# Kernel tuning notes

Measured on AMD Instinct MI355X. Metric: run time of the kernel, lower is better.

The kernel has to match this reference:

```python
import jax, jax.numpy as jnp
import numpy as np

N_NODES = 50000
N_EDGES = 1_250_000
D = 64
L = 3

def setup_inputs() -> dict:
    key = jax.random.key(0)
    k1, k2, k3, k4, k5, k6 = jax.random.split(key, 6)
    h = jax.random.normal(k1, (N_NODES, D), dtype=jnp.float32)
    edge_weight = jax.random.uniform(k2, (N_EDGES,), dtype=jnp.float32)
    # Glorot-ish scale keeps tanh in its responsive range
    Ws = jax.random.normal(k3, (L, D, D), dtype=jnp.float32) * (1.0 / np.sqrt(D))
    bs = jax.random.normal(k4, (L, D), dtype=jnp.float32) * 0.01
    src = jax.random.randint(k5, (N_EDGES,), 0, N_NODES, dtype=jnp.int64 if jax.config.jax_enable_x64 else jnp.int32)
    dst = jax.random.randint(k6, (N_EDGES,), 0, N_NODES, dtype=jnp.int64 if jax.config.jax_enable_x64 else jnp.int32)
    return {"h": h, "edge_weight": edge_weight, "Ws": Ws, "bs": bs, "src": src, "dst": dst}

def reference(h, edge_weight, Ws, bs, src, dst):
    # Stacked DGL GraphConv(norm='none'), edge-weighted: aggregate-then-transform
    # (in_feats == out_feats, so DGL aggregates first), tanh between layers,
    # concat of all intermediate representations along feature dim.
    n = h.shape[0]
    results = [h]
    for i in range(L):
        msg = h[src] * edge_weight[:, None]            # [E, D] gather-scale
        agg = jax.ops.segment_sum(msg, dst, num_segments=n)  # [N, D] scatter-add
        h = agg @ Ws[i] + bs[i]                        # dense transform + bias
        if i != L - 1:
            h = jnp.tanh(h)
        results.append(h)
    return jnp.concatenate(results, axis=1)           # [N, (L+1)*D]
```

## Files before the change

kernel.cpp:

```cpp
#include <hip/hip_runtime.h>
#include <hip/hip_fp16.h>
#include <math.h>

#define N_NODES 50000
#define N_EDGES 1250000
#define D 64
#define OUTC 256
#define CAP 64
#define SCAN_BLOCKS ((N_NODES + 255) / 256)

#define WSB_CNT      0
#define WSB_BUCKET   802816
#define WSB_H16_0    13602816
#define WSB_H16_1    20002816
#define WS_BUCKET_NEEDED 26402816

#define WS_DEG      0
#define WS_FILL     204800
#define WS_ROWPTR   409600
#define WS_BSUM     609664
#define WS_BOFF     610496
#define WS_EDGES    614400
#define WS_H16_0    10616832
#define WS_H16_1    (WS_H16_0 + (size_t)N_NODES * D * 2)
#define WS_F16_NEEDED (WS_H16_1 + (size_t)N_NODES * D * 2)
#define WS_CSR_NEEDED (WS_EDGES + (size_t)N_EDGES * 8)


#define PREP_T (50000 + 800000)
__global__ __launch_bounds__(256) void prep_kernel(const float* __restrict__ h,
                                                   float* __restrict__ out,
                                                   __half* __restrict__ h16,
                                                   int4* __restrict__ cnt4) {
    int tid = blockIdx.x * 256 + threadIdx.x;
    if (tid < 50000) { cnt4[tid] = make_int4(0, 0, 0, 0); return; }
    tid -= 50000;
    if (tid >= 800000) return;
    int row = tid >> 4;
    int c4  = tid & 15;
    float4 v = ((const float4*)h)[tid];
    ((float4*)(out + (size_t)row * OUTC))[c4] = v;
    __half2* p = (__half2*)(h16 + (size_t)row * D + c4 * 4);
    p[0] = __floats2half2_rn(v.x, v.y);
    p[1] = __floats2half2_rn(v.z, v.w);
}

#define FILL_GBLK 611
__global__ __launch_bounds__(256) void bucket_fill_kernel(const int* __restrict__ src,
                                                          const int* __restrict__ dst,
                                                          const float* __restrict__ ew,
                                                          int* __restrict__ cnt,
                                                          unsigned* __restrict__ bucket) {
    int p = blockIdx.x & 7;
    int g = blockIdx.x >> 3;
    int nlo = p * 6250, nhi = nlo + 6250;
    int e0 = (g * 256 + threadIdx.x) * 8;
    if (e0 >= N_EDGES) return;
    int4   d0 = *(const int4*)(dst + e0);
    int4   d1 = *(const int4*)(dst + e0 + 4);
    int4   s0 = *(const int4*)(src + e0);
    int4   s1 = *(const int4*)(src + e0 + 4);
    float4 w0 = *(const float4*)(ew + e0);
    float4 w1 = *(const float4*)(ew + e0 + 4);
    int   dd[8] = {d0.x, d0.y, d0.z, d0.w, d1.x, d1.y, d1.z, d1.w};
    int   ss[8] = {s0.x, s0.y, s0.z, s0.w, s1.x, s1.y, s1.z, s1.w};
    float ww[8] = {w0.x, w0.y, w0.z, w0.w, w1.x, w1.y, w1.z, w1.w};
#pragma unroll
    for (int i = 0; i < 8; i++) {
        int d = dd[i];
        if (d >= nlo && d < nhi) {
            int c = atomicAdd(&cnt[d * 4], 1) & (CAP - 1);
            unsigned hw = (unsigned)__half_as_ushort(__float2half(ww[i]));
            bucket[(size_t)d * CAP + c] = ((unsigned)ss[i] << 16) | hw;
        }
    }
}


#define WGEMM_BLOCKS 782
__global__ __launch_bounds__(256) void wgemm_kernel(__half* __restrict__ xy,
                                                    const float* __restrict__ W) {
    int t = threadIdx.x, lane = t & 63, wv = t >> 6;
    float Wreg[D];
#pragma unroll
    for (int k = 0; k < D; k++) Wreg[k] = W[k * D + lane];
    int row0 = blockIdx.x * 64 + wv * 16;
#pragma unroll 1
    for (int r = 0; r < 16; r++) {
        int row = row0 + r;
        if (row >= N_NODES) break;
        const __half2* __restrict__ xr = (const __half2*)(xy + (size_t)row * D);
        float o = 0.0f;
#pragma unroll
        for (int j = 0; j < 32; j++) {
            float2 x2 = __half22float2(xr[j]);
            o = fmaf(x2.x, Wreg[2 * j],     o);
            o = fmaf(x2.y, Wreg[2 * j + 1], o);
        }
        xy[(size_t)row * D + lane] = __float2half(o);
    }
}

#define AGG_BLOCKS 12500
__global__ __launch_bounds__(256) void agg_kernel(const __half* __restrict__ y16,
                                                  const unsigned* __restrict__ bucket,
                                                  const int* __restrict__ cnt,
                                                  const float* __restrict__ bias,
                                                  float* __restrict__ hout,
                                                  __half* __restrict__ h16out,
                                                  int apply_tanh) {
    int t = threadIdx.x, lane = t & 63, wv = t >> 6;
    int fb = lane & 7;
    int eo = lane >> 3;
    const uint4* __restrict__ h4 = (const uint4*)y16;

    int n  = __builtin_amdgcn_readfirstlane(blockIdx.x * 4 + wv);
    int cn = cnt[n * 4];
    const uint4* bp4 = (const uint4*)(bucket + (size_t)n * CAP);
    uint4 qqa = bp4[eo];
    cn = __builtin_amdgcn_readfirstlane(cn > CAP ? CAP : cn);
    int off2 = (cn > 32) ? 8 : 0;
    uint4 qqb = bp4[off2 + eo];

    float acc[8];
#pragma unroll
    for (int u = 0; u < 8; u++) acc[u] = 0.0f;

    auto processChunk = [&](uint4 qq, int j) {
        int sbase = j + eo * 4;
        unsigned ee[4];
        ee[0] = (sbase + 0 < cn) ? qq.x : 0u;
        ee[1] = (sbase + 1 < cn) ? qq.y : 0u;
        ee[2] = (sbase + 2 < cn) ? qq.z : 0u;
        ee[3] = (sbase + 3 < cn) ? qq.w : 0u;
        uint4 g[4];
#pragma unroll
        for (int i = 0; i < 4; i++)
            g[i] = h4[(size_t)(ee[i] >> 16) * 8 + fb];
#pragma unroll
        for (int i = 0; i < 4; i++) {
            float w = __half2float(__ushort_as_half((unsigned short)(ee[i] & 0xFFFFu)));
            const __half2* hv = (const __half2*)&g[i];
#pragma unroll
            for (int tt = 0; tt < 4; tt++) {
                float2 f2 = __half22float2(hv[tt]);
                acc[2 * tt]     = fmaf(f2.x, w, acc[2 * tt]);
                acc[2 * tt + 1] = fmaf(f2.y, w, acc[2 * tt + 1]);
            }
        }
    };

    processChunk(qqa, 0);
    if (cn > 32) processChunk(qqb, 32);

    int b0 = (lane >> 3) & 1, b1 = (lane >> 4) & 1, b2 = (lane >> 5) & 1;
    float k1[4];
#pragma unroll
    for (int j = 0; j < 4; j++) {
        float send = b0 ? acc[2 * j] : acc[2 * j + 1];
        float keep = b0 ? acc[2 * j + 1] : acc[2 * j];
        k1[j] = keep + __shfl_xor(send, 8);
    }
    float k2[2];
#pragma unroll
    for (int j = 0; j < 2; j++) {
        float send = b1 ? k1[2 * j] : k1[2 * j + 1];
        float keep = b1 ? k1[2 * j + 1] : k1[2 * j];
        k2[j] = keep + __shfl_xor(send, 16);
    }
    float send = b2 ? k2[0] : k2[1];
    float keep = b2 ? k2[1] : k2[0];
    float o = keep + __shfl_xor(send, 32);

    int f = (fb << 3) | eo;
    o += bias[f];
    if (apply_tanh) o = tanhf(o);
    hout[(size_t)n * OUTC + f] = o;
    if (h16out) h16out[(size_t)n * D + f] = __float2half(o);
}


__global__ __launch_bounds__(256) void copy_h_kernel(const float* __restrict__ h,
                                                     float* __restrict__ out,
                                                     __half* __restrict__ h16) {
    int idx = blockIdx.x * 256 + threadIdx.x;
    if (idx >= N_NODES * D / 4) return;
    int row = idx >> 4;
    int c4  = idx & 15;
    float4 v = ((const float4*)h)[idx];
    ((float4*)(out + (size_t)row * OUTC))[c4] = v;
    if (h16) {
        __half2* p = (__half2*)(h16 + (size_t)row * D + c4 * 4);
        p[0] = __floats2half2_rn(v.x, v.y);
        p[1] = __floats2half2_rn(v.z, v.w);
    }
}

__global__ __launch_bounds__(256) void hist_kernel(const int* __restrict__ dst,
                                                   int* __restrict__ deg) {
    int e = blockIdx.x * 256 + threadIdx.x;
    if (e >= N_EDGES) return;
    atomicAdd(&deg[dst[e]], 1);
}

__global__ __launch_bounds__(256) void scan_partial_kernel(const int* __restrict__ deg,
                                                           int* __restrict__ bsum) {
    __shared__ int ws4[4];
    int t = threadIdx.x;
    int i = blockIdx.x * 256 + t;
    int v = (i < N_NODES) ? deg[i] : 0;
#pragma unroll
    for (int off = 32; off >= 1; off >>= 1) v += __shfl_xor(v, off);
    if ((t & 63) == 0) ws4[t >> 6] = v;
    __syncthreads();
    if (t == 0) bsum[blockIdx.x] = ws4[0] + ws4[1] + ws4[2] + ws4[3];
}

__global__ __launch_bounds__(256) void scan_bsum_kernel(const int* __restrict__ bsum,
                                                        int* __restrict__ boff,
                                                        int* __restrict__ row_ptr) {
    __shared__ int wsum[4];
    int t = threadIdx.x, lane = t & 63, w = t >> 6;
    int v = (t < SCAN_BLOCKS) ? bsum[t] : 0;
    int x = v;
#pragma unroll
    for (int off = 1; off < 64; off <<= 1) {
        int y = __shfl_up(x, off);
        if (lane >= off) x += y;
    }
    if (lane == 63) wsum[w] = x;
    __syncthreads();
    int wo = 0;
    for (int u = 0; u < w; u++) wo += wsum[u];
    int excl = wo + x - v;
    if (t < SCAN_BLOCKS) boff[t] = excl;
    if (t == SCAN_BLOCKS - 1) row_ptr[N_NODES] = excl + v;
}

__global__ __launch_bounds__(256) void scan_final_kernel(const int* __restrict__ deg,
                                                         const int* __restrict__ boff,
                                                         int* __restrict__ row_ptr) {
    __shared__ int wsum[4];
    int t = threadIdx.x, lane = t & 63, w = t >> 6;
    int i = blockIdx.x * 256 + t;
    int v = (i < N_NODES) ? deg[i] : 0;
    int x = v;
#pragma unroll
    for (int off = 1; off < 64; off <<= 1) {
        int y = __shfl_up(x, off);
        if (lane >= off) x += y;
    }
    if (lane == 63) wsum[w] = x;
    __syncthreads();
    int wo = 0;
    for (int u = 0; u < w; u++) wo += wsum[u];
    if (i < N_NODES) row_ptr[i] = boff[blockIdx.x] + wo + (x - v);
}

__global__ __launch_bounds__(256) void fill_kernel(const int* __restrict__ src,
                                                   const int* __restrict__ dst,
                                                   const float* __restrict__ ew,
                                                   const int* __restrict__ row_ptr,
                                                   int* __restrict__ fill,
                                                   int2* __restrict__ edges) {
    int e = blockIdx.x * 256 + threadIdx.x;
    if (e >= N_EDGES) return;
    int d = dst[e];
    int p = atomicAdd(&fill[d], 1);
    edges[row_ptr[d] + p] = make_int2(src[e], __float_as_int(ew[e]));
}

#define LAYER_BLOCKS 3125
__global__ __launch_bounds__(256) void layer2_kernel(const __half* __restrict__ h16src,
                                                     const int2* __restrict__ edges,
                                                     const int* __restrict__ row_ptr,
                                                     const float* __restrict__ W,
                                                     const float* __restrict__ bias,
                                                     float* __restrict__ hout,
                                                     __half* __restrict__ h16out,
                                                     int apply_tanh) {
    __shared__ float Wlds[D * D];
    int t = threadIdx.x, lane = t & 63, wv = t >> 6;
    for (int i = t; i < D * D; i += 256) Wlds[i] = W[i];
    __syncthreads();
    int p  = lane & 31;
    int hh = lane >> 5;
    const __half2* __restrict__ h2 = (const __half2*)h16src;
    float bv = bias[lane];
    int waveId = blockIdx.x * 4 + wv;
    for (int n0 = waveId; n0 < N_NODES; n0 += LAYER_BLOCKS * 4) {
        int n = __builtin_amdgcn_readfirstlane(n0);
        int beg = __builtin_amdgcn_readfirstlane(row_ptr[n]);
        int end = __builtin_amdgcn_readfirstlane(row_ptr[n + 1]);
        float2 acc = make_float2(0.0f, 0.0f);
        int j = beg;
        for (; j + 8 <= end; j += 8) {
            int2 a0 = edges[j + 0], a1 = edges[j + 1];
            int2 a2 = edges[j + 2], a3 = edges[j + 3];
            int2 a4 = edges[j + 4], a5 = edges[j + 5];
            int2 a6 = edges[j + 6], a7 = edges[j + 7];
            int   s0 = hh ? a1.x : a0.x;  float w0 = __int_as_float(hh ? a1.y : a0.y);
            int   s1 = hh ? a3.x : a2.x;  float w1 = __int_as_float(hh ? a3.y : a2.y);
            int   s2 = hh ? a5.x : a4.x;  float w2 = __int_as_float(hh ? a5.y : a4.y);
            int   s3 = hh ? a7.x : a6.x;  float w3 = __int_as_float(hh ? a7.y : a6.y);
            __half2 v0 = h2[(size_t)s0 * 32 + p];
            __half2 v1 = h2[(size_t)s1 * 32 + p];
            __half2 v2 = h2[(size_t)s2 * 32 + p];
            __half2 v3 = h2[(size_t)s3 * 32 + p];
            acc.x = fmaf(__low2float(v0), w0, acc.x);  acc.y = fmaf(__high2float(v0), w0, acc.y);
            acc.x = fmaf(__low2float(v1), w1, acc.x);  acc.y = fmaf(__high2float(v1), w1, acc.y);
            acc.x = fmaf(__low2float(v2), w2, acc.x);  acc.y = fmaf(__high2float(v2), w2, acc.y);
            acc.x = fmaf(__low2float(v3), w3, acc.x);  acc.y = fmaf(__high2float(v3), w3, acc.y);
        }
        for (; j + 2 <= end; j += 2) {
            int2 a0 = edges[j], a1 = edges[j + 1];
            int   s0 = hh ? a1.x : a0.x;  float w0 = __int_as_float(hh ? a1.y : a0.y);
            __half2 v0 = h2[(size_t)s0 * 32 + p];
            acc.x = fmaf(__low2float(v0), w0, acc.x);  acc.y = fmaf(__high2float(v0), w0, acc.y);
        }
        if (j < end) {
            int2 a0 = edges[j];
            float w0 = hh ? 0.0f : __int_as_float(a0.y);
            __half2 v0 = h2[(size_t)a0.x * 32 + p];
            acc.x = fmaf(__low2float(v0), w0, acc.x);  acc.y = fmaf(__high2float(v0), w0, acc.y);
        }
        acc.x += __shfl_xor(acc.x, 32);
        acc.y += __shfl_xor(acc.y, 32);
        float o0 = bv, o1 = 0.f, o2 = 0.f, o3 = 0.f;
#pragma unroll
        for (int k = 0; k < D; k += 4) {
            int q = k >> 1;
            o0 = fmaf(__shfl(acc.x, q),     Wlds[(k + 0) * D + lane], o0);
            o1 = fmaf(__shfl(acc.y, q),     Wlds[(k + 1) * D + lane], o1);
            o2 = fmaf(__shfl(acc.x, q + 1), Wlds[(k + 2) * D + lane], o2);
            o3 = fmaf(__shfl(acc.y, q + 1), Wlds[(k + 3) * D + lane], o3);
        }
        float o = (o0 + o1) + (o2 + o3);
        if (apply_tanh) o = tanhf(o);
        hout[(size_t)n * OUTC + lane] = o;
        if (h16out) h16out[(size_t)n * D + lane] = __float2half(o);
    }
}

__global__ __launch_bounds__(256) void scatter_kernel(const float* __restrict__ hin,
                                                      const float* __restrict__ ew,
                                                      const int* __restrict__ src,
                                                      const int* __restrict__ dst,
                                                      float* __restrict__ agg) {
    long long gid = (long long)blockIdx.x * 256 + threadIdx.x;
    int e = (int)(gid >> 6);
    int lane = (int)(gid & 63);
    if (e >= N_EDGES) return;
    float v = hin[(size_t)src[e] * OUTC + lane] * ew[e];
    atomicAdd(&agg[(size_t)dst[e] * OUTC + lane], v);
}

__global__ __launch_bounds__(256) void gemm_kernel(float* __restrict__ hio,
                                                   const float* __restrict__ W,
                                                   const float* __restrict__ bias,
                                                   int apply_tanh) {
    __shared__ float Wl[D][D + 1];
    __shared__ float rowbuf[4][D];
    int t = threadIdx.x;
    for (int i = t; i < D * D; i += 256) Wl[i >> 6][i & (D - 1)] = W[i];
    int r = t >> 6, c = t & (D - 1);
    float bv = bias[c];
    int row0 = blockIdx.x * 64;
    for (int rr = 0; rr < 64; rr += 4) {
        int row = row0 + rr + r;
        __syncthreads();
        rowbuf[r][c] = (row < N_NODES) ? hio[(size_t)row * OUTC + c] : 0.0f;
        __syncthreads();
        float acc = bv;
#pragma unroll
        for (int k = 0; k < D; k++) acc = fmaf(rowbuf[r][k], Wl[k][c], acc);
        if (apply_tanh) acc = tanhf(acc);
        if (row < N_NODES) hio[(size_t)row * OUTC + c] = acc;
    }
}

extern "C" void kernel_launch(void* const* d_in, const int* in_sizes, int n_in,
                              void* d_out, int out_size, void* d_ws, size_t ws_size,
                              hipStream_t stream) {
    const float* h   = (const float*)d_in[0];
    const float* ew  = (const float*)d_in[1];
    const float* Ws  = (const float*)d_in[2];
    const float* bs  = (const float*)d_in[3];
    const int*   src = (const int*)d_in[4];
    const int*   dst = (const int*)d_in[5];
    float* out = (float*)d_out;

    if (ws_size >= WS_BUCKET_NEEDED) {
        char* ws = (char*)d_ws;
        int*      cnt    = (int*)(ws + WSB_CNT);
        unsigned* bucket = (unsigned*)(ws + WSB_BUCKET);
        __half*   h16a   = (__half*)(ws + WSB_H16_0);
        __half*   h16b   = (__half*)(ws + WSB_H16_1);

        prep_kernel<<<(PREP_T + 255) / 256, 256, 0, stream>>>(
            h, out, h16a, (int4*)cnt);
        bucket_fill_kernel<<<FILL_GBLK * 8, 256, 0, stream>>>(
            src, dst, ew, cnt, bucket);
        __half* cur = h16a;
        __half* nxt = h16b;
        for (int i = 0; i < 3; i++) {
            wgemm_kernel<<<WGEMM_BLOCKS, 256, 0, stream>>>(cur, Ws + (size_t)i * D * D);
            agg_kernel<<<AGG_BLOCKS, 256, 0, stream>>>(
                cur, bucket, cnt, bs + (size_t)i * D,
                out + (size_t)(i + 1) * D,
                (i == 2) ? nullptr : nxt, (i < 2) ? 1 : 0);
            __half* tmp = cur; cur = nxt; nxt = tmp;
        }
    } else if (ws_size >= WS_CSR_NEEDED) {
        char* ws = (char*)d_ws;
        int*  deg     = (int*)(ws + WS_DEG);
        int*  fillc   = (int*)(ws + WS_FILL);
        int*  row_ptr = (int*)(ws + WS_ROWPTR);
        int*  bsum    = (int*)(ws + WS_BSUM);
        int*  boff    = (int*)(ws + WS_BOFF);
        int2* edges   = (int2*)(ws + WS_EDGES);
        bool use_f16 = (ws_size >= WS_F16_NEEDED);
        __half* h16a = use_f16 ? (__half*)(ws + WS_H16_0) : nullptr;
        __half* h16b = use_f16 ? (__half*)(ws + WS_H16_1) : nullptr;

        hipMemsetAsync(ws, 0, WS_ROWPTR, stream);
        copy_h_kernel<<<(N_NODES * D / 4 + 255) / 256, 256, 0, stream>>>(h, out, h16a);
        hist_kernel<<<(N_EDGES + 255) / 256, 256, 0, stream>>>(dst, deg);
        scan_partial_kernel<<<SCAN_BLOCKS, 256, 0, stream>>>(deg, bsum);
        scan_bsum_kernel<<<1, 256, 0, stream>>>(bsum, boff, row_ptr);
        scan_final_kernel<<<SCAN_BLOCKS, 256, 0, stream>>>(deg, boff, row_ptr);
        fill_kernel<<<(N_EDGES + 255) / 256, 256, 0, stream>>>(src, dst, ew, row_ptr, fillc, edges);
        for (int i = 0; i < 3; i++) {
            float* hout = out + (size_t)(i + 1) * D;
            __half* hsrc = (i & 1) ? h16b : h16a;
            __half* hdst = (i == 2) ? nullptr : ((i & 1) ? h16a : h16b);
            layer2_kernel<<<LAYER_BLOCKS, 256, 0, stream>>>(
                hsrc, edges, row_ptr, Ws + (size_t)i * D * D, bs + (size_t)i * D,
                hout, hdst, (i < 2) ? 1 : 0);
        }
    } else {
        hipMemsetAsync(out, 0, (size_t)N_NODES * OUTC * sizeof(float), stream);
        copy_h_kernel<<<(N_NODES * D / 4 + 255) / 256, 256, 0, stream>>>(h, out, nullptr);
        for (int i = 0; i < 3; i++) {
            const float* hin = out + (size_t)i * D;
            float*       agg = out + (size_t)(i + 1) * D;
            long long nthreads = (long long)N_EDGES * 64;
            scatter_kernel<<<(int)((nthreads + 255) / 256), 256, 0, stream>>>(hin, ew, src, dst, agg);
            gemm_kernel<<<(N_NODES + 63) / 64, 256, 0, stream>>>(
                agg, Ws + (size_t)i * D * D, bs + (size_t)i * D, (i < 2) ? 1 : 0);
        }
    }
}
```

Baseline: 273.7 us.

## Switch to aggregate-then-transform with a split-feature aggregation kernel and fused fill/copy

Reorders each layer to aggregate first and then run the dense transform. Bias, tanh and the output write move into the GEMM kernel. The aggregation kernel is rewritten so two blocks each cover half the features of a node, with a loop over 16-edge passes that uses non-temporal bucket loads. The prep and bucket-fill kernels are merged into one launch, and the counter zeroing becomes a memset. This trades transform-then-aggregate for more gather lanes per node and fewer launches, at the cost of an extra fp16 intermediate round trip and changed rounding order.

New measurement: 330.0 us. 1.21x slower.

```diff
diff --git a/kernel.cpp b/kernel.cpp
--- a/kernel.cpp
+++ b/kernel.cpp
@@ -27,156 +27,144 @@
 #define WS_CSR_NEEDED (WS_EDGES + (size_t)N_EDGES * 8)
 
 
-#define PREP_T (50000 + 800000)
-__global__ __launch_bounds__(256) void prep_kernel(const float* __restrict__ h,
-                                                   float* __restrict__ out,
-                                                   __half* __restrict__ h16,
-                                                   int4* __restrict__ cnt4) {
-    int tid = blockIdx.x * 256 + threadIdx.x;
-    if (tid < 50000) { cnt4[tid] = make_int4(0, 0, 0, 0); return; }
-    tid -= 50000;
-    if (tid >= 800000) return;
-    int row = tid >> 4;
-    int c4  = tid & 15;
-    float4 v = ((const float4*)h)[tid];
-    ((float4*)(out + (size_t)row * OUTC))[c4] = v;
-    __half2* p = (__half2*)(h16 + (size_t)row * D + c4 * 4);
-    p[0] = __floats2half2_rn(v.x, v.y);
-    p[1] = __floats2half2_rn(v.z, v.w);
-}
-
-#define FILL_GBLK 611
-__global__ __launch_bounds__(256) void bucket_fill_kernel(const int* __restrict__ src,
-                                                          const int* __restrict__ dst,
-                                                          const float* __restrict__ ew,
-                                                          int* __restrict__ cnt,
-                                                          unsigned* __restrict__ bucket) {
-    int p = blockIdx.x & 7;
-    int g = blockIdx.x >> 3;
-    int nlo = p * 6250, nhi = nlo + 6250;
-    int e0 = (g * 256 + threadIdx.x) * 8;
-    if (e0 >= N_EDGES) return;
-    int4   d0 = *(const int4*)(dst + e0);
-    int4   d1 = *(const int4*)(dst + e0 + 4);
-    int4   s0 = *(const int4*)(src + e0);
-    int4   s1 = *(const int4*)(src + e0 + 4);
-    float4 w0 = *(const float4*)(ew + e0);
-    float4 w1 = *(const float4*)(ew + e0 + 4);
-    int   dd[8] = {d0.x, d0.y, d0.z, d0.w, d1.x, d1.y, d1.z, d1.w};
-    int   ss[8] = {s0.x, s0.y, s0.z, s0.w, s1.x, s1.y, s1.z, s1.w};
-    float ww[8] = {w0.x, w0.y, w0.z, w0.w, w1.x, w1.y, w1.z, w1.w};
-#pragma unroll
-    for (int i = 0; i < 8; i++) {
-        int d = dd[i];
-        if (d >= nlo && d < nhi) {
-            int c = atomicAdd(&cnt[d * 4], 1) & (CAP - 1);
-            unsigned hw = (unsigned)__half_as_ushort(__float2half(ww[i]));
-            bucket[(size_t)d * CAP + c] = ((unsigned)ss[i] << 16) | hw;
-        }
-    }
-}
-
-
-#define WGEMM_BLOCKS 782
-__global__ __launch_bounds__(256) void wgemm_kernel(__half* __restrict__ xy,
-                                                    const float* __restrict__ W) {
+#define FILLCOPY_FILLB 4888
+#define FILLCOPY_COPYB 3125
+__global__ __launch_bounds__(256) void fillcopy_kernel(const int* __restrict__ src,
+                                                       const int* __restrict__ dst,
+                                                       const float* __restrict__ ew,
+                                                       int* __restrict__ cnt,
+                                                       unsigned* __restrict__ bucket,
+                                                       const float* __restrict__ h,
+                                                       float* __restrict__ out,
+                                                       __half* __restrict__ h16) {
+    if (blockIdx.x < FILLCOPY_FILLB) {
+        int p = blockIdx.x & 7;
+        int g = blockIdx.x >> 3;
+        int nlo = p * 6250, nhi = nlo + 6250;
+        int e0 = (g * 256 + threadIdx.x) * 8;
+        if (e0 >= N_EDGES) return;
+        int4   d0 = *(const int4*)(dst + e0);
+        int4   d1 = *(const int4*)(dst + e0 + 4);
+        int4   s0 = *(const int4*)(src + e0);
+        int4   s1 = *(const int4*)(src + e0 + 4);
+        float4 w0 = *(const float4*)(ew + e0);
+        float4 w1 = *(const float4*)(ew + e0 + 4);
+        int   dd[8] = {d0.x, d0.y, d0.z, d0.w, d1.x, d1.y, d1.z, d1.w};
+        int   ss[8] = {s0.x, s0.y, s0.z, s0.w, s1.x, s1.y, s1.z, s1.w};
+        float ww[8] = {w0.x, w0.y, w0.z, w0.w, w1.x, w1.y, w1.z, w1.w};
+#pragma unroll
+        for (int i = 0; i < 8; i++) {
+            int d = dd[i];
+            if (d >= nlo && d < nhi) {
+                int c = atomicAdd(&cnt[d * 4], 1) & (CAP - 1);
+                unsigned hw = (unsigned)__half_as_ushort(__float2half(ww[i]));
+                bucket[(size_t)d * CAP + c] = ((unsigned)ss[i] << 16) | hw;
+            }
+        }
+    } else {
+        int tid = (blockIdx.x - FILLCOPY_FILLB) * 256 + threadIdx.x;
+        if (tid >= 800000) return;
+        int row = tid >> 4;
+        int c4  = tid & 15;
+        float4 v = ((const float4*)h)[tid];
+        ((float4*)(out + (size_t)row * OUTC))[c4] = v;
+        __half2* pp = (__half2*)(h16 + (size_t)row * D + c4 * 4);
+        pp[0] = __floats2half2_rn(v.x, v.y);
+        pp[1] = __floats2half2_rn(v.z, v.w);
+    }
+}
+
+
+#define AGG2_BLOCKS 25000
+__global__ __launch_bounds__(256) void agg2_kernel(const __half* __restrict__ cur,
+                                                   const unsigned* __restrict__ bucket,
+                                                   const int* __restrict__ cnt,
+                                                   __half* __restrict__ agg16) {
+    int t = threadIdx.x, lane = t & 63, wv = t >> 6;
+    int g  = blockIdx.x & 1;
+    int n  = __builtin_amdgcn_readfirstlane((blockIdx.x >> 1) * 4 + wv);
+    int fc = lane & 3;
+    int cn_raw = cnt[n * 4];
+    int cn = __builtin_amdgcn_readfirstlane(cn_raw > CAP ? CAP : cn_raw);
+    const unsigned* bp = bucket + (size_t)n * CAP;
+    const uint4* __restrict__ h4 = (const uint4*)cur;
+    int gbase = g * 4 + fc;
+
+    float acc[8];
+#pragma unroll
+    for (int u = 0; u < 8; u++) acc[u] = 0.0f;
+
+    int npass = (cn + 15) >> 4;
+    for (int p = 0; p < npass; p++) {
+        int slot = p * 16 + (lane >> 2);
+        unsigned qq = __builtin_nontemporal_load(&bp[slot]);
+        qq = (slot < cn) ? qq : 0u;
+        uint4 gv = h4[(size_t)(qq >> 16) * 8 + gbase];
+        float w = __half2float(__ushort_as_half((unsigned short)(qq & 0xFFFFu)));
+        const __half2* hv = (const __half2*)&gv;
+#pragma unroll
+        for (int tt = 0; tt < 4; tt++) {
+            float2 f2 = __half22float2(hv[tt]);
+            acc[2 * tt]     = fmaf(f2.x, w, acc[2 * tt]);
+            acc[2 * tt + 1] = fmaf(f2.y, w, acc[2 * tt + 1]);
+        }
+    }
+
+    int b0 = (lane >> 2) & 1, b1 = (lane >> 3) & 1, b2 = (lane >> 4) & 1;
+    float k1[4];
+#pragma unroll
+    for (int j = 0; j < 4; j++) {
+        float send = b0 ? acc[2 * j] : acc[2 * j + 1];
+        float keep = b0 ? acc[2 * j + 1] : acc[2 * j];
+        k1[j] = keep + __shfl_xor(send, 4);
+    }
+    float k2[2];
+#pragma unroll
+    for (int j = 0; j < 2; j++) {
+        float send = b1 ? k1[2 * j] : k1[2 * j + 1];
+        float keep = b1 ? k1[2 * j + 1] : k1[2 * j];
+        k2[j] = keep + __shfl_xor(send, 8);
+    }
+    float send = b2 ? k2[0] : k2[1];
+    float keep = b2 ? k2[1] : k2[0];
+    float v = keep + __shfl_xor(send, 16);
+    v = v + __shfl_xor(v, 32);
+
+    if (lane < 32) {
+        int u = b0 + 2 * b1 + 4 * b2;
+        agg16[(size_t)n * D + g * 32 + fc * 8 + u] = __float2half(v);
+    }
+}
+
+#define WGEMM2_BLOCKS 782
+__global__ __launch_bounds__(256) void wgemm2_kernel(__half* __restrict__ xy,
+                                                     const float* __restrict__ W,
+                                                     const float* __restrict__ bias,
+                                                     float* __restrict__ outcol,
+                                                     int apply_tanh,
+                                                     int write_h16) {
     int t = threadIdx.x, lane = t & 63, wv = t >> 6;
     float Wreg[D];
 #pragma unroll
     for (int k = 0; k < D; k++) Wreg[k] = W[k * D + lane];
+    float bv = bias[lane];
     int row0 = blockIdx.x * 64 + wv * 16;
 #pragma unroll 1
     for (int r = 0; r < 16; r++) {
         int row = row0 + r;
         if (row >= N_NODES) break;
         const __half2* __restrict__ xr = (const __half2*)(xy + (size_t)row * D);
-        float o = 0.0f;
+        float o = bv;
 #pragma unroll
         for (int j = 0; j < 32; j++) {
             float2 x2 = __half22float2(xr[j]);
             o = fmaf(x2.x, Wreg[2 * j],     o);
             o = fmaf(x2.y, Wreg[2 * j + 1], o);
         }
-        xy[(size_t)row * D + lane] = __float2half(o);
-    }
-}
-
-#define AGG_BLOCKS 12500
-__global__ __launch_bounds__(256) void agg_kernel(const __half* __restrict__ y16,
-                                                  const unsigned* __restrict__ bucket,
-                                                  const int* __restrict__ cnt,
-                                                  const float* __restrict__ bias,
-                                                  float* __restrict__ hout,
-                                                  __half* __restrict__ h16out,
-                                                  int apply_tanh) {
-    int t = threadIdx.x, lane = t & 63, wv = t >> 6;
-    int fb = lane & 7;
-    int eo = lane >> 3;
-    const uint4* __restrict__ h4 = (const uint4*)y16;
-
-    int n  = __builtin_amdgcn_readfirstlane(blockIdx.x * 4 + wv);
-    int cn = cnt[n * 4];
-    const uint4* bp4 = (const uint4*)(bucket + (size_t)n * CAP);
-    uint4 qqa = bp4[eo];
-    cn = __builtin_amdgcn_readfirstlane(cn > CAP ? CAP : cn);
-    int off2 = (cn > 32) ? 8 : 0;
-    uint4 qqb = bp4[off2 + eo];
-
-    float acc[8];
-#pragma unroll
-    for (int u = 0; u < 8; u++) acc[u] = 0.0f;
-
-    auto processChunk = [&](uint4 qq, int j) {
-        int sbase = j + eo * 4;
-        unsigned ee[4];
-        ee[0] = (sbase + 0 < cn) ? qq.x : 0u;
-        ee[1] = (sbase + 1 < cn) ? qq.y : 0u;
-        ee[2] = (sbase + 2 < cn) ? qq.z : 0u;
-        ee[3] = (sbase + 3 < cn) ? qq.w : 0u;
-        uint4 g[4];
-#pragma unroll
-        for (int i = 0; i < 4; i++)
-            g[i] = h4[(size_t)(ee[i] >> 16) * 8 + fb];
-#pragma unroll
-        for (int i = 0; i < 4; i++) {
-            float w = __half2float(__ushort_as_half((unsigned short)(ee[i] & 0xFFFFu)));
-            const __half2* hv = (const __half2*)&g[i];
-#pragma unroll
-            for (int tt = 0; tt < 4; tt++) {
-                float2 f2 = __half22float2(hv[tt]);
-                acc[2 * tt]     = fmaf(f2.x, w, acc[2 * tt]);
-                acc[2 * tt + 1] = fmaf(f2.y, w, acc[2 * tt + 1]);
-            }
-        }
-    };
-
-    processChunk(qqa, 0);
-    if (cn > 32) processChunk(qqb, 32);
-
-    int b0 = (lane >> 3) & 1, b1 = (lane >> 4) & 1, b2 = (lane >> 5) & 1;
-    float k1[4];
-#pragma unroll
-    for (int j = 0; j < 4; j++) {
-        float send = b0 ? acc[2 * j] : acc[2 * j + 1];
-        float keep = b0 ? acc[2 * j + 1] : acc[2 * j];
-        k1[j] = keep + __shfl_xor(send, 8);
-    }
-    float k2[2];
-#pragma unroll
-    for (int j = 0; j < 2; j++) {
-        float send = b1 ? k1[2 * j] : k1[2 * j + 1];
-        float keep = b1 ? k1[2 * j + 1] : k1[2 * j];
-        k2[j] = keep + __shfl_xor(send, 16);
-    }
-    float send = b2 ? k2[0] : k2[1];
-    float keep = b2 ? k2[1] : k2[0];
-    float o = keep + __shfl_xor(send, 32);
-
-    int f = (fb << 3) | eo;
-    o += bias[f];
-    if (apply_tanh) o = tanhf(o);
-    hout[(size_t)n * OUTC + f] = o;
-    if (h16out) h16out[(size_t)n * D + f] = __float2half(o);
+        if (apply_tanh) o = tanhf(o);
+        outcol[(size_t)row * OUTC + lane] = o;
+        if (write_h16) xy[(size_t)row * D + lane] = __float2half(o);
+    }
 }
 
 
@@ -397,18 +385,16 @@
         __half*   h16a   = (__half*)(ws + WSB_H16_0);
         __half*   h16b   = (__half*)(ws + WSB_H16_1);
 
-        prep_kernel<<<(PREP_T + 255) / 256, 256, 0, stream>>>(
-            h, out, h16a, (int4*)cnt);
-        bucket_fill_kernel<<<FILL_GBLK * 8, 256, 0, stream>>>(
-            src, dst, ew, cnt, bucket);
+        hipMemsetAsync(cnt, 0, 800000, stream);
+        fillcopy_kernel<<<FILLCOPY_FILLB + FILLCOPY_COPYB, 256, 0, stream>>>(
+            src, dst, ew, cnt, bucket, h, out, h16a);
         __half* cur = h16a;
         __half* nxt = h16b;
         for (int i = 0; i < 3; i++) {
-            wgemm_kernel<<<WGEMM_BLOCKS, 256, 0, stream>>>(cur, Ws + (size_t)i * D * D);
-            agg_kernel<<<AGG_BLOCKS, 256, 0, stream>>>(
-                cur, bucket, cnt, bs + (size_t)i * D,
-                out + (size_t)(i + 1) * D,
-                (i == 2) ? nullptr : nxt, (i < 2) ? 1 : 0);
+            agg2_kernel<<<AGG2_BLOCKS, 256, 0, stream>>>(cur, bucket, cnt, nxt);
+            wgemm2_kernel<<<WGEMM2_BLOCKS, 256, 0, stream>>>(
+                nxt, Ws + (size_t)i * D * D, bs + (size_t)i * D,
+                out + (size_t)(i + 1) * D, (i < 2) ? 1 : 0, (i < 2) ? 1 : 0);
             __half* tmp = cur; cur = nxt; nxt = tmp;
         }
     } else if (ws_size >= WS_CSR_NEEDED) {
```
